# Kernel tuning notes

Measured on AMD Instinct MI355X. Metric: run time of the kernel, lower is better.

The kernel has to match this reference:

```python
import jax, jax.numpy as jnp
import numpy as np

TAU = 2.0      # LIF membrane time constant
VTH = 1.0      # spiking threshold (spikingjelly default)
ALPHA = 4.0    # surrogate sigmoid sharpness (spikingjelly Sigmoid default)
EPS = 1e-5     # BatchNorm eps


@jax.custom_vjp
def spike(v):
    # Heaviside(v) with surrogate sigmoid gradient
    return (v >= 0.0).astype(v.dtype)

def _spike_fwd(v):
    return spike(v), v

def _spike_bwd(v, g):
    s = jax.nn.sigmoid(ALPHA * v)
    return (g * ALPHA * s * (1.0 - s),)

spike.defvjp(_spike_fwd, _spike_bwd)


def lif(x_seq):
    # MultiStepLIFNode: x_seq [T, B, C], v_reset=0 (hard reset), detach_reset=True
    def step(v, xt):
        v = v + (xt - v) / TAU           # membrane decay + charge
        s = spike(v - VTH)               # fire
        v = v * (1.0 - jax.lax.stop_gradient(s))  # detached hard reset to 0
        return v, s
    v0 = jnp.zeros_like(x_seq[0])
    _, s_seq = jax.lax.scan(step, v0, x_seq)
    return s_seq


def block(h, w, b, gamma, beta):
    # h: [B, C_in, T] -> conv1d(k=3, pad=1) -> BN (batch stats) -> LIF -> [B, E, T]
    y = jax.lax.conv_general_dilated(h, w, window_strides=(1,), padding=[(1, 1)],
                                     dimension_numbers=('NCH', 'OIH', 'NCH'))
    y = y + b[None, :, None]
    mu = y.mean(axis=(0, 2), keepdims=True)
    var = y.var(axis=(0, 2), keepdims=True)
    y = (y - mu) * jax.lax.rsqrt(var + EPS) * gamma[None, :, None] + beta[None, :, None]
    s = lif(jnp.transpose(y, (2, 0, 1)))        # [T, B, E]
    return jnp.transpose(s, (1, 2, 0))          # [B, E, T]


def setup_inputs() -> dict:
    key = jax.random.key(0)
    ks = jax.random.split(key, 8)
    B, T, Cin, E, O = 64, 1024, 8, 256, 63
    return {
        'x':       jax.random.normal(ks[0], (B, T, Cin), jnp.float32),
        'conv0_w': jax.random.normal(ks[1], (E, Cin, 3), jnp.float32) * (1.0 / np.sqrt(Cin * 3)),
        'conv0_b': jax.random.normal(ks[2], (E,), jnp.float32) * 0.01,
        'convs_w': jax.random.normal(ks[3], (3, E, E, 3), jnp.float32) * (1.0 / np.sqrt(E * 3)),
        'convs_b': jax.random.normal(ks[4], (3, E), jnp.float32) * 0.01,
        'bn_gamma': jnp.ones((4, E), jnp.float32),
        'bn_beta':  jnp.zeros((4, E), jnp.float32),
        'head_w':  jax.random.normal(ks[5], (O, E), jnp.float32) * (1.0 / np.sqrt(E)),
        'head_b':  jnp.zeros((O,), jnp.float32),
    }


def reference(x, conv0_w, conv0_b, convs_w, convs_b, bn_gamma, bn_beta, head_w, head_b):
    h = jnp.transpose(x, (0, 2, 1))  # [B, C, T]
    h = block(h, conv0_w, conv0_b, bn_gamma[0], bn_beta[0])
    for i in range(convs_w.shape[0]):
        h = block(h, convs_w[i], convs_b[i], bn_gamma[i + 1], bn_beta[i + 1])
    h = h.mean(axis=-1)  # AdaptiveAvgPool1d(1) + squeeze -> [B, E]
    return h @ head_w.T + head_b  # [B, O]
```

## Files before the change

kernel.cpp:

```cpp
#include <hip/hip_runtime.h>
#include <hip/hip_bf16.h>
#include <stdint.h>

#define NB 64
#define NT 1024
#define CIN 8
#define NE 256
#define NO 63
#define TPAD 16
#define TROWS (NT + 2*TPAD)
#define LCH 128
#define LWU 48
#define TT 256

using bf16x8 = __attribute__((ext_vector_type(8))) short;
using f32x4  = __attribute__((ext_vector_type(4))) float;


__global__ void conv0_prep(const float* __restrict__ x, const float* __restrict__ w0,
                           const float* __restrict__ b0, float* __restrict__ y,
                           double* __restrict__ acc0,
                           const float* __restrict__ cw, __hip_bfloat16* __restrict__ wfr) {
    int bid = blockIdx.x;
    if (bid >= 512) {
        int F = (bid - 512) * 256 + threadIdx.x;
        int lane = F & 63;
        int xx = F >> 6;
        int cph = xx & 7;  xx >>= 3;
        int e4  = xx & 15; xx >>= 4;
        int s   = xx & 1;  xx >>= 1;
        int k   = xx % 3;
        int l   = xx / 3;
        int e = e4*16 + (lane & 15);
        int cb = cph*32 + (lane >> 4)*8;
        __hip_bfloat16 outv[8];
        #pragma unroll
        for (int j = 0; j < 8; ++j) {
            float w = cw[((size_t)(l*256 + e)*256 + (cb + j))*3 + k];
            __hip_bfloat16 hi = __float2bfloat16(w);
            if (s == 0) outv[j] = hi;
            else        outv[j] = __float2bfloat16(w - __bfloat162float(hi));
        }
        *(uint4*)(wfr + (size_t)F*8) = *(uint4*)outv;
        return;
    }
    int b = bid >> 3, tc = bid & 7;
    int e = threadIdx.x;
    int t0 = tc * 128;
    __shared__ float xs[1040];
    for (int i = threadIdx.x; i < 1040; i += 256) {
        int t = t0 - 1 + (i >> 3); int c = i & 7;
        xs[i] = (t >= 0 && t < NT) ? x[((size_t)b*NT + t)*CIN + c] : 0.0f;
    }
    __syncthreads();
    float w[24];
    #pragma unroll
    for (int j = 0; j < 24; ++j) w[j] = w0[e*24 + j];
    float bias = b0[e];
    float s = 0.0f, qq = 0.0f;
    for (int dt = 0; dt < 128; ++dt) {
        float acc = bias;
        #pragma unroll
        for (int c = 0; c < 8; ++c)
            #pragma unroll
            for (int k = 0; k < 3; ++k)
                acc += xs[(dt + k)*8 + c] * w[c*3 + k];
        y[((size_t)b*NT + t0 + dt)*NE + e] = acc;
        s += acc; qq += acc*acc;
    }
    atomicAdd(&acc0[e],       (double)s);
    atomicAdd(&acc0[256 + e], (double)qq);
}

template<bool WS>
__global__ void lif_kern(const float* __restrict__ y, const double* __restrict__ acc,
                         const float* __restrict__ gamma, const float* __restrict__ beta,
                         __hip_bfloat16* __restrict__ S, float* __restrict__ pool) {
    int c = blockIdx.x, b = blockIdx.y;
    int e = threadIdx.x;
    double sa = acc[e], qa = acc[256 + e];
    double mean = sa * (1.0/65536.0);
    double var  = qa * (1.0/65536.0) - mean*mean;
    float rs  = (float)(1.0 / sqrt(var + 1e-5));
    float mu  = (float)mean;
    float rsg = rs * gamma[e];
    float bet = beta[e];
    const __hip_bfloat16 z   = __float2bfloat16(0.0f);
    const __hip_bfloat16 one = __float2bfloat16(1.0f);
    if (WS) {
        if (c == 0) {
            for (int r = 0; r < TPAD; ++r) S[((size_t)b*TROWS + r)*NE + e] = z;
        }
        if (c == 7) {
            for (int r = 0; r < TPAD; ++r) S[((size_t)b*TROWS + TPAD + NT + r)*NE + e] = z;
        }
    }
    int t0 = c * LCH;
    int tw = t0 - LWU; if (tw < 0) tw = 0;
    const float* yb = y + (size_t)b*NT*NE + e;
    __hip_bfloat16* sb = S + ((size_t)b*TROWS + TPAD)*NE + e;
    float v = 0.0f;
    #pragma unroll 8
    for (int t = tw; t < t0; ++t) {
        float xx = yb[(size_t)t*NE];
        float yn = (xx - mu)*rsg + bet;
        float d  = __fsub_rn(yn, v);
        v = __fadd_rn(v, __fmul_rn(d, 0.5f));
        v = (v >= 1.0f) ? 0.0f : v;
    }
    float cnt = 0.0f;
    #pragma unroll 8
    for (int t = t0; t < t0 + LCH; ++t) {
        float xx = yb[(size_t)t*NE];
        float yn = (xx - mu)*rsg + bet;
        float d  = __fsub_rn(yn, v);
        v = __fadd_rn(v, __fmul_rn(d, 0.5f));
        bool sp = (v >= 1.0f);
        if (WS) sb[(size_t)t*NE] = sp ? one : z;
        else    cnt += sp ? 1.0f : 0.0f;
        v = sp ? 0.0f : v;
    }
    if (!WS) pool[(size_t)(b*8 + c)*256 + e] = cnt;
}

__global__ __launch_bounds__(256, 2) void conv_mfma(
    const __hip_bfloat16* __restrict__ Sp,
    const __hip_bfloat16* __restrict__ Wfr,
    const float* __restrict__ bias,
    float* __restrict__ y,
    double* __restrict__ acc_out)
{
    __shared__ short Bbuf[260*32];
    __shared__ short Abuf[48*512];
    const int tid  = threadIdx.x;
    const int wave = tid >> 6, lane = tid & 63;
    const int n16  = lane & 15, q = lane >> 4;
    const int we = wave & 1, wt = wave >> 1;
    const int tt = blockIdx.x, et = blockIdx.y, b = blockIdx.z;
    const int t0 = tt * TT;

    f32x4 acc[4][8] = {};
    bf16x8 bfr[8];

    const __hip_bfloat16* Sbase = Sp + ((size_t)b*TROWS + (TPAD - 1 + t0)) * NE;

    for (int ph = 0; ph < 8; ++ph) {
        const int c0 = ph * 32;
        __syncthreads();
        for (int idx = tid; idx < 258*4; idx += 256) {
            int r = idx >> 2, sg = idx & 3;
            uint4 d = *(const uint4*)(Sbase + (size_t)r*NE + c0 + sg*8);
            int sgs = sg ^ ((r >> 1) & 3);
            *(uint4*)((char*)Bbuf + r*64 + sgs*16) = d;
        }
        #pragma unroll
        for (int it = 0; it < 12; ++it) {
            int idx = tid + it*256;
            int chunk = idx >> 6, li = idx & 63;
            int ks = chunk >> 3, e4i = chunk & 7;
            const __hip_bfloat16* src = Wfr + ((((size_t)ks*16 + et*8 + e4i)*8 + ph) << 9) + li*8;
            uint4 d = *(const uint4*)src;
            *(uint4*)(Abuf + chunk*512 + li*8) = d;
        }
        __syncthreads();
        #pragma unroll 1
        for (int kk = 0; kk < 3; ++kk) {
            #pragma unroll
            for (int g = 0; g < 8; ++g) {
                int row = wt*128 + g*16 + n16 + kk;
                int sgs = q ^ ((row >> 1) & 3);
                bfr[g] = *(const bf16x8*)((const char*)Bbuf + row*64 + sgs*16);
            }
            #pragma unroll
            for (int s = 0; s < 2; ++s) {
                const short* ab = Abuf + ((kk*2 + s)*8 + we*4)*512 + lane*8;
                bf16x8 afr[4];
                #pragma unroll
                for (int f = 0; f < 4; ++f)
                    afr[f] = *(const bf16x8*)(ab + f*512);
                #pragma unroll
                for (int f = 0; f < 4; ++f)
                    #pragma unroll
                    for (int g = 0; g < 8; ++g)
                        acc[f][g] = __builtin_amdgcn_mfma_f32_16x16x32_bf16(afr[f], bfr[g], acc[f][g], 0, 0, 0);
            }
        }
    }

    float ls[16], lq[16];
    #pragma unroll
    for (int f = 0; f < 4; ++f) {
        int e_loc = et*128 + we*64 + f*16 + q*4;
        float4 bv = *(const float4*)(bias + e_loc);
        float s0=0,s1=0,s2=0,s3=0, q0=0,q1=0,q2=0,q3=0;
        #pragma unroll
        for (int g = 0; g < 8; ++g) {
            int t = t0 + wt*128 + g*16 + n16;
            f32x4 a = acc[f][g];
            float4 o;
            o.x = a[0] + bv.x; o.y = a[1] + bv.y; o.z = a[2] + bv.z; o.w = a[3] + bv.w;
            *(float4*)(y + ((size_t)b*NT + t)*NE + e_loc) = o;
            s0 += o.x; q0 += o.x*o.x;
            s1 += o.y; q1 += o.y*o.y;
            s2 += o.z; q2 += o.z*o.z;
            s3 += o.w; q3 += o.w*o.w;
        }
        ls[f*4+0]=s0; lq[f*4+0]=q0;
        ls[f*4+1]=s1; lq[f*4+1]=q1;
        ls[f*4+2]=s2; lq[f*4+2]=q2;
        ls[f*4+3]=s3; lq[f*4+3]=q3;
    }
    #pragma unroll
    for (int off = 1; off < 16; off <<= 1) {
        #pragma unroll
        for (int i = 0; i < 16; ++i) {
            ls[i] += __shfl_xor(ls[i], off, 64);
            lq[i] += __shfl_xor(lq[i], off, 64);
        }
    }
    __syncthreads();
    float* red = (float*)Bbuf;
    if (n16 == 0 && wt == 0) {
        #pragma unroll
        for (int f = 0; f < 4; ++f)
            #pragma unroll
            for (int r = 0; r < 4; ++r) {
                int el = we*64 + f*16 + q*4 + r;
                red[el] = ls[f*4+r]; red[128+el] = lq[f*4+r];
            }
    }
    __syncthreads();
    if (n16 == 0 && wt == 1) {
        #pragma unroll
        for (int f = 0; f < 4; ++f)
            #pragma unroll
            for (int r = 0; r < 4; ++r) {
                int el = we*64 + f*16 + q*4 + r;
                red[el] += ls[f*4+r]; red[128+el] += lq[f*4+r];
            }
    }
    __syncthreads();
    if (tid < 128) {
        int e = et*128 + tid;
        atomicAdd(&acc_out[e],       (double)red[tid]);
        atomicAdd(&acc_out[256 + e], (double)red[128 + tid]);
    }
}

__global__ void head_final(const float* __restrict__ pool, const float* __restrict__ hw,
                           const float* __restrict__ hb, float* __restrict__ out) {
    int b = blockIdx.x;
    int tid = threadIdx.x;
    __shared__ float pooled[256];
    float s = 0.0f;
    #pragma unroll
    for (int c = 0; c < 8; ++c) s += pool[(size_t)(b*8 + c)*256 + tid];
    pooled[tid] = s * (1.0f/1024.0f);
    __syncthreads();
    if (tid < NO) {
        float acc = hb[tid];
        for (int c = 0; c < 256; ++c) acc += pooled[c] * hw[tid*256 + c];
        out[b*NO + tid] = acc;
    }
}

extern "C" void kernel_launch(void* const* d_in, const int* in_sizes, int n_in,
                              void* d_out, int out_size, void* d_ws, size_t ws_size,
                              hipStream_t stream) {
    (void)in_sizes; (void)n_in; (void)out_size; (void)ws_size;
    const float* x       = (const float*)d_in[0];
    const float* conv0_w = (const float*)d_in[1];
    const float* conv0_b = (const float*)d_in[2];
    const float* convs_w = (const float*)d_in[3];
    const float* convs_b = (const float*)d_in[4];
    const float* bn_g    = (const float*)d_in[5];
    const float* bn_b    = (const float*)d_in[6];
    const float* head_w  = (const float*)d_in[7];
    const float* head_b  = (const float*)d_in[8];
    float* out = (float*)d_out;

    char* ws = (char*)d_ws;
    float*          y    = (float*)ws;
    __hip_bfloat16* S    = (__hip_bfloat16*)(ws + 67108864);
    __hip_bfloat16* Wfr  = (__hip_bfloat16*)(ws + 101711872);
    double*         acc  = (double*)(ws + 104071168);
    float*          pool = (float*)(ws + 104087552);

    conv0_prep<<<1088, 256, 0, stream>>>(x, conv0_w, conv0_b, y, acc, convs_w, Wfr);
    lif_kern<true><<<dim3(8, 64), 256, 0, stream>>>(y, acc, bn_g, bn_b, S, nullptr);

    for (int l = 0; l < 3; ++l) {
        conv_mfma<<<dim3(4, 2, 64), 256, 0, stream>>>(S, Wfr + (size_t)l*393216,
                                                      convs_b + l*256, y, acc + (l+1)*512);
        const float* g = bn_g + (l+1)*256;
        const float* bb = bn_b + (l+1)*256;
        if (l < 2) lif_kern<true ><<<dim3(8, 64), 256, 0, stream>>>(y, acc + (l+1)*512, g, bb, S, nullptr);
        else       lif_kern<false><<<dim3(8, 64), 256, 0, stream>>>(y, acc + (l+1)*512, g, bb, S, pool);
    }
    head_final<<<64, 256, 0, stream>>>(pool, head_w, head_b, out);
}
```

Baseline: 337.5 us.

## Double-buffer spike tiles via direct global-to-LDS loads; read weights from global

The conv MFMA kernel now stages the spike (B operand) tiles into two LDS buffers with global_load_lds, prefetching the next channel phase while the current one computes, so only one barrier is needed per phase. The weight fragments are no longer copied into LDS and are loaded straight from global memory (relying on cache) into registers before each MFMA batch. s_setprio is raised around the MFMA bursts. This removes the LDS staging round-trip and the serialized load/compute per phase, at the cost of global-latency exposure on the A fragments and a larger B buffer footprint.

```diff
diff --git a/kernel.cpp b/kernel.cpp
--- a/kernel.cpp
+++ b/kernel.cpp
@@ -15,6 +15,7 @@
 
 using bf16x8 = __attribute__((ext_vector_type(8))) short;
 using f32x4  = __attribute__((ext_vector_type(4))) float;
+typedef unsigned int u32;
 
 
 __global__ void conv0_prep(const float* __restrict__ x, const float* __restrict__ w0,
@@ -130,8 +131,7 @@
     float* __restrict__ y,
     double* __restrict__ acc_out)
 {
-    __shared__ short Bbuf[260*32];
-    __shared__ short Abuf[48*512];
+    __shared__ short Bbuf[2][272*32];
     const int tid  = threadIdx.x;
     const int wave = tid >> 6, lane = tid & 63;
     const int n16  = lane & 15, q = lane >> 4;
@@ -144,47 +144,53 @@
 
     const __hip_bfloat16* Sbase = Sp + ((size_t)b*TROWS + (TPAD - 1 + t0)) * NE;
 
+    auto stage = [&](int buf, int c0) {
+        for (int ch = wave; ch < 17; ch += 4) {
+            int r  = ch*16 + (lane >> 2);
+            int sg = (lane & 3) ^ ((r >> 1) & 3);
+            const __hip_bfloat16* src = Sbase + (size_t)r*NE + c0 + sg*8;
+            char* dst = (char*)(&Bbuf[0][0]) + buf*17408 + ch*1024;
+            __builtin_amdgcn_global_load_lds(
+                (const __attribute__((address_space(1))) u32*)src,
+                (__attribute__((address_space(3))) u32*)dst, 16, 0, 0);
+        }
+    };
+
+    stage(0, 0);
+    asm volatile("s_waitcnt vmcnt(0)" ::: "memory");
+    __syncthreads();
+
     for (int ph = 0; ph < 8; ++ph) {
-        const int c0 = ph * 32;
-        __syncthreads();
-        for (int idx = tid; idx < 258*4; idx += 256) {
-            int r = idx >> 2, sg = idx & 3;
-            uint4 d = *(const uint4*)(Sbase + (size_t)r*NE + c0 + sg*8);
-            int sgs = sg ^ ((r >> 1) & 3);
-            *(uint4*)((char*)Bbuf + r*64 + sgs*16) = d;
-        }
-        #pragma unroll
-        for (int it = 0; it < 12; ++it) {
-            int idx = tid + it*256;
-            int chunk = idx >> 6, li = idx & 63;
-            int ks = chunk >> 3, e4i = chunk & 7;
-            const __hip_bfloat16* src = Wfr + ((((size_t)ks*16 + et*8 + e4i)*8 + ph) << 9) + li*8;
-            uint4 d = *(const uint4*)src;
-            *(uint4*)(Abuf + chunk*512 + li*8) = d;
-        }
-        __syncthreads();
+        const int buf = ph & 1;
+        if (ph < 7) stage(buf ^ 1, (ph + 1) * 32);
+        const short* Bb = &Bbuf[buf][0];
         #pragma unroll 1
         for (int kk = 0; kk < 3; ++kk) {
             #pragma unroll
             for (int g = 0; g < 8; ++g) {
                 int row = wt*128 + g*16 + n16 + kk;
                 int sgs = q ^ ((row >> 1) & 3);
-                bfr[g] = *(const bf16x8*)((const char*)Bbuf + row*64 + sgs*16);
+                bfr[g] = *(const bf16x8*)((const char*)Bb + row*64 + sgs*16);
             }
             #pragma unroll
             for (int s = 0; s < 2; ++s) {
-                const short* ab = Abuf + ((kk*2 + s)*8 + we*4)*512 + lane*8;
+                const __hip_bfloat16* ab =
+                    Wfr + ((((size_t)(kk*2 + s)*16 + et*8 + we*4)*8 + ph) << 9) + lane*8;
                 bf16x8 afr[4];
                 #pragma unroll
                 for (int f = 0; f < 4; ++f)
-                    afr[f] = *(const bf16x8*)(ab + f*512);
+                    afr[f] = *(const bf16x8*)(ab + (size_t)f*4096);
+                __builtin_amdgcn_s_setprio(1);
                 #pragma unroll
                 for (int f = 0; f < 4; ++f)
                     #pragma unroll
                     for (int g = 0; g < 8; ++g)
                         acc[f][g] = __builtin_amdgcn_mfma_f32_16x16x32_bf16(afr[f], bfr[g], acc[f][g], 0, 0, 0);
+                __builtin_amdgcn_s_setprio(0);
             }
         }
+        asm volatile("s_waitcnt vmcnt(0)" ::: "memory");
+        __syncthreads();
     }
 
     float ls[16], lq[16];
@@ -219,7 +225,7 @@
         }
     }
     __syncthreads();
-    float* red = (float*)Bbuf;
+    float* red = (float*)(&Bbuf[0][0]);
     if (n16 == 0 && wt == 0) {
         #pragma unroll
         for (int f = 0; f < 4; ++f)
```

Result: no change. 336.8 us (-0.2%).
